# Kernel tuning notes

Hardware: AMD Instinct MI355X
Metric: run time of the kernel (lower is better)

Reference implementation:

```python
import jax, jax.numpy as jnp
import numpy as np

N_NODES = 10000
N_EDGES = 160000
D = 512            # input_dim = hidden_size = output_dim
NUM_EXPERTS = 4
N_LAYERS = 2


def setup_inputs() -> dict:
    key = jax.random.key(0)
    k = jax.random.split(key, 7)
    x = jax.random.normal(k[0], (N_NODES, D), dtype=jnp.float32)
    edge_index = jax.random.randint(k[1], (2, N_EDGES), 0, N_NODES, dtype=jnp.int32)
    # Gating network (Linear D -> NUM_EXPERTS)
    gate_w = jax.random.normal(k[2], (D, NUM_EXPERTS), dtype=jnp.float32) * 0.05
    gate_b = jnp.zeros((NUM_EXPERTS,), dtype=jnp.float32)
    # Per-expert SAGEConv weights: lin_r (self/root) and lin_l (neighbor) + bias
    w_self = jax.random.normal(k[3], (NUM_EXPERTS, N_LAYERS, D, D), dtype=jnp.float32) * 0.05
    w_neigh = jax.random.normal(k[4], (NUM_EXPERTS, N_LAYERS, D, D), dtype=jnp.float32) * 0.05
    b_exp = jnp.zeros((NUM_EXPERTS, N_LAYERS, D), dtype=jnp.float32)
    return {"x": x, "edge_index": edge_index, "gate_w": gate_w, "gate_b": gate_b,
            "w_self": w_self, "w_neigh": w_neigh, "b_exp": b_exp, "top_k": 1}


def reference(x, edge_index, gate_w, gate_b, w_self, w_neigh, b_exp, top_k):
    n = x.shape[0]
    src, dst = edge_index[0], edge_index[1]
    # mean-aggregation normalization (PyG SAGEConv aggr='mean'); 0 for isolated nodes
    deg = jax.ops.segment_sum(jnp.ones_like(src, dtype=x.dtype), dst, num_segments=n)
    inv_deg = jnp.where(deg > 0, 1.0 / jnp.maximum(deg, 1.0), 0.0)[:, None]  # [N,1]

    # gating: softmax(Linear(x)) then top-k routing
    gate = jax.nn.softmax(x @ gate_w + gate_b, axis=-1)          # [N, E]
    top_vals, top_idx = jax.lax.top_k(gate, top_k)               # [N, k]

    def expert(ws, wn, b):  # ws, wn: [L, D, D]; b: [L, D]
        h = x
        for l in range(N_LAYERS):
            agg = jax.ops.segment_sum(h[src], dst, num_segments=n) * inv_deg
            # SAGEConv: lin_l(mean_neigh) + lin_r(x) + bias, then relu (norm='id', eval dropout)
            h = jax.nn.relu(agg @ wn[l] + h @ ws[l] + b[l])
        return h

    # dense all-expert compute (matches original module)
    outs = jax.vmap(expert)(w_self, w_neigh, b_exp)              # [E, N, D]
    outs = jnp.transpose(outs, (1, 0, 2))                        # [N, E, D]
    sel = jnp.take_along_axis(outs, top_idx[:, :, None], axis=1)  # [N, k, D]
    return jnp.sum(sel * top_vals[:, :, None], axis=1)           # [N, D]
```

## Files before the change

### kernel.cpp

```cpp
#include <hip/hip_runtime.h>
#include <hip/hip_bf16.h>
#include <cstdint>

#define N_NODES 10000
#define N_EDGES 160000
#define DIM 512
#define K1 1024
#define NEXP 4

typedef __bf16 bf16_t;
typedef bf16_t bf16x8 __attribute__((ext_vector_type(8)));
typedef float f32x4 __attribute__((ext_vector_type(4)));

#define AS1(p) ((__attribute__((address_space(1))) void*)(p))
#define AS3(p) ((__attribute__((address_space(3))) void*)(p))

__global__ void zero_kernel(int* __restrict__ deg, int* __restrict__ ecnt) {
    int i = blockIdx.x * blockDim.x + threadIdx.x;
    if (i < N_NODES) deg[i] = 0;
    if (i < NEXP) ecnt[i] = 0;
}

__global__ void gate_kernel(const float* __restrict__ x,
                            const float* __restrict__ gw,
                            const float* __restrict__ gb,
                            int* __restrict__ top_idx,
                            float* __restrict__ top_val,
                            bf16_t* __restrict__ acat) {
    const int wave = threadIdx.x >> 6;
    const int lane = threadIdx.x & 63;
    const int node = blockIdx.x * 4 + wave;
    if (node >= N_NODES) return;
    const float4* x4 = (const float4*)(x + (size_t)node * DIM);
    const float4* gw4 = (const float4*)gw;
    float4 xa = x4[lane * 2];
    float4 xb = x4[lane * 2 + 1];
    float xv[8] = { xa.x, xa.y, xa.z, xa.w, xb.x, xb.y, xb.z, xb.w };
    float a0 = 0.f, a1 = 0.f, a2 = 0.f, a3 = 0.f;
    #pragma unroll
    for (int c = 0; c < 8; c++) {
        float4 g = gw4[lane * 8 + c];
        a0 += xv[c] * g.x; a1 += xv[c] * g.y; a2 += xv[c] * g.z; a3 += xv[c] * g.w;
    }
    bf16x8 o;
    #pragma unroll
    for (int c = 0; c < 8; c++) o[c] = (bf16_t)xv[c];
    *(bf16x8*)(acat + (size_t)node * K1 + DIM + lane * 8) = o;
    for (int off = 32; off > 0; off >>= 1) {
        a0 += __shfl_xor(a0, off);
        a1 += __shfl_xor(a1, off);
        a2 += __shfl_xor(a2, off);
        a3 += __shfl_xor(a3, off);
    }
    if (lane == 0) {
        float z[4] = { a0 + gb[0], a1 + gb[1], a2 + gb[2], a3 + gb[3] };
        int bi = 0; float bm = z[0];
        for (int e = 1; e < 4; e++) if (z[e] > bm) { bm = z[e]; bi = e; }
        float den = 0.f;
        for (int e = 0; e < 4; e++) den += expf(z[e] - bm);
        top_idx[node] = bi;
        top_val[node] = 1.0f / den;
    }
}

__global__ void bucket_kernel(const int* __restrict__ top_idx,
                              int* __restrict__ ecnt,
                              int* __restrict__ lists) {
    __shared__ int lcnt[NEXP];
    __shared__ int base[NEXP];
    const int tid = threadIdx.x;
    if (tid < NEXP) lcnt[tid] = 0;
    __syncthreads();
    const int node = blockIdx.x * 256 + tid;
    int e = 0, rank = 0;
    if (node < N_NODES) {
        e = top_idx[node];
        rank = atomicAdd(&lcnt[e], 1);
    }
    __syncthreads();
    if (tid < NEXP) base[tid] = atomicAdd(&ecnt[tid], lcnt[tid]);
    __syncthreads();
    if (node < N_NODES) lists[e * N_NODES + base[e] + rank] = node;
}

__global__ void deg_kernel(const int* __restrict__ dst, int* __restrict__ deg) {
    int i = blockIdx.x * blockDim.x + threadIdx.x;
    if (i < N_EDGES) atomicAdd(&deg[dst[i]], 1);
}

__global__ void scan_kernel(const int* __restrict__ deg,
                            int* __restrict__ offs,
                            int* __restrict__ cursor) {
    __shared__ int wsum[16];
    __shared__ int carrysh;
    const int tid = threadIdx.x;
    const int lane = tid & 63;
    const int wv = tid >> 6;
    if (tid == 0) carrysh = 0;
    __syncthreads();
    for (int base = 0; base < N_NODES; base += 1024) {
        int i = base + tid;
        int v = (i < N_NODES) ? deg[i] : 0;
        int s = v;
        #pragma unroll
        for (int off = 1; off < 64; off <<= 1) {
            int t = __shfl_up(s, off);
            if (lane >= off) s += t;
        }
        if (lane == 63) wsum[wv] = s;
        int carry = carrysh;
        __syncthreads();
        if (wv == 0) {
            int w = (lane < 16) ? wsum[lane] : 0;
            #pragma unroll
            for (int off = 1; off < 16; off <<= 1) {
                int t = __shfl_up(w, off);
                if (lane >= off) w += t;
            }
            if (lane < 16) wsum[lane] = w;
        }
        __syncthreads();
        int wbase = (wv > 0) ? wsum[wv - 1] : 0;
        int excl = carry + wbase + s - v;
        if (i < N_NODES) { offs[i] = excl; cursor[i] = excl; }
        int total = wsum[15];
        __syncthreads();
        if (tid == 0) carrysh = carry + total;
        __syncthreads();
    }
    if (tid == 0) offs[N_NODES] = carrysh;
}

__global__ void fill_kernel(const int* __restrict__ src, const int* __restrict__ dst,
                            int* __restrict__ cursor, int* __restrict__ csr) {
    int i = blockIdx.x * blockDim.x + threadIdx.x;
    if (i < N_EDGES) {
        int d = dst[i];
        int p = atomicAdd(&cursor[d], 1);
        csr[p] = src[i];
    }
}

__global__ void wtrans_kernel(const float* __restrict__ w_neigh,
                              const float* __restrict__ w_self,
                              bf16_t* __restrict__ Bt) {
    __shared__ float tile[32][33];
    const int m = blockIdx.z;
    const bool isSelf = m >= 8;
    const int el = m & 7;
    const float* W = (isSelf ? w_self : w_neigh) + (size_t)el * DIM * DIM;
    const int k0 = blockIdx.x * 32;
    const int n0 = blockIdx.y * 32;
    const int tx = threadIdx.x, ty = threadIdx.y;
    for (int r = ty; r < 32; r += 8)
        tile[r][tx] = W[(size_t)(k0 + r) * DIM + n0 + tx];
    __syncthreads();
    for (int r = ty; r < 32; r += 8) {
        int n = n0 + r;
        int k = k0 + tx;
        Bt[((size_t)el * DIM + n) * K1 + (isSelf ? DIM : 0) + k] = (bf16_t)tile[tx][r];
    }
}

__global__ void agg1_kernel(const int* __restrict__ offs, const int* __restrict__ csr,
                            bf16_t* __restrict__ acat) {
    const int wave = threadIdx.x >> 6;
    const int lane = threadIdx.x & 63;
    const int node = blockIdx.x * 4 + wave;
    if (node >= N_NODES) return;
    const int c0 = lane * 8;
    float s[8] = {0,0,0,0,0,0,0,0};
    int beg = offs[node];
    int end = offs[node + 1];
    int d = end - beg;
    int p = beg;
    for (; p + 8 <= end; p += 8) {
        bf16x8 v[8];
        #pragma unroll
        for (int q = 0; q < 8; q++) {
            int idx = csr[p + q];
            v[q] = *(const bf16x8*)(acat + (size_t)idx * K1 + DIM + c0);
        }
        #pragma unroll
        for (int q = 0; q < 8; q++)
            #pragma unroll
            for (int k = 0; k < 8; k++) s[k] += (float)v[q][k];
    }
    for (; p + 4 <= end; p += 4) {
        bf16x8 v[4];
        #pragma unroll
        for (int q = 0; q < 4; q++) {
            int idx = csr[p + q];
            v[q] = *(const bf16x8*)(acat + (size_t)idx * K1 + DIM + c0);
        }
        #pragma unroll
        for (int q = 0; q < 4; q++)
            #pragma unroll
            for (int k = 0; k < 8; k++) s[k] += (float)v[q][k];
    }
    for (; p < end; p++) {
        int idx = csr[p];
        bf16x8 v0 = *(const bf16x8*)(acat + (size_t)idx * K1 + DIM + c0);
        #pragma unroll
        for (int k = 0; k < 8; k++) s[k] += (float)v0[k];
    }
    float w = d > 0 ? 1.0f / (float)d : 0.0f;
    bf16x8 o;
    #pragma unroll
    for (int k = 0; k < 8; k++) o[k] = (bf16_t)(s[k] * w);
    *(bf16x8*)(acat + (size_t)node * K1 + c0) = o;
}

__global__ void agg2_kernel(const int* __restrict__ offs, const int* __restrict__ csr,
                            const int* __restrict__ top_idx,
                            const bf16_t* __restrict__ h1, bf16_t* __restrict__ acat) {
    const int wave = threadIdx.x >> 6;
    const int lane = threadIdx.x & 63;
    const int node = blockIdx.x * 4 + wave;
    if (node >= N_NODES) return;
    const int c0 = lane * 8;
    const bf16_t* hb = h1 + (size_t)top_idx[node] * N_NODES * DIM;
    float s[8] = {0,0,0,0,0,0,0,0};
    int beg = offs[node];
    int end = offs[node + 1];
    int d = end - beg;
    int p = beg;
    for (; p + 8 <= end; p += 8) {
        bf16x8 v[8];
        #pragma unroll
        for (int q = 0; q < 8; q++) {
            int idx = csr[p + q];
            v[q] = *(const bf16x8*)(hb + (size_t)idx * DIM + c0);
        }
        #pragma unroll
        for (int q = 0; q < 8; q++)
            #pragma unroll
            for (int k = 0; k < 8; k++) s[k] += (float)v[q][k];
    }
    for (; p + 4 <= end; p += 4) {
        bf16x8 v[4];
        #pragma unroll
        for (int q = 0; q < 4; q++) {
            int idx = csr[p + q];
            v[q] = *(const bf16x8*)(hb + (size_t)idx * DIM + c0);
        }
        #pragma unroll
        for (int q = 0; q < 4; q++)
            #pragma unroll
            for (int k = 0; k < 8; k++) s[k] += (float)v[q][k];
    }
    for (; p < end; p++) {
        int idx = csr[p];
        bf16x8 v0 = *(const bf16x8*)(hb + (size_t)idx * DIM + c0);
        #pragma unroll
        for (int k = 0; k < 8; k++) s[k] += (float)v0[k];
    }
    float w = d > 0 ? 1.0f / (float)d : 0.0f;
    bf16x8 o;
    #pragma unroll
    for (int k = 0; k < 8; k++) o[k] = (bf16_t)(s[k] * w);
    *(bf16x8*)(acat + (size_t)node * K1 + c0) = o;
    *(bf16x8*)(acat + (size_t)node * K1 + DIM + c0) = *(const bf16x8*)(hb + (size_t)node * DIM + c0);
}

template <int MODE>
__global__ __launch_bounds__(256)
void gemm_kernel(const bf16_t* __restrict__ A,
                 const bf16_t* __restrict__ Bt,
                 const int layer,
                 const float* __restrict__ bias_all,
                 bf16_t* __restrict__ h1,
                 float* __restrict__ out,
                 const int* __restrict__ lists,
                 const int* __restrict__ ecnt,
                 const float* __restrict__ top_val) {
    int bx, by, e;
    if (MODE == 0) {
        const int b = blockIdx.x;
        const int kq = b & 7;
        const int ke = kq >> 2;
        const int ky = kq & 3;
        const int r = b >> 3;
        const int yloc = r >> 3;
        const int xz = r & 7;
        bx = xz & 3;
        e = ke * 2 + (xz >> 2);
        by = ky * 20 + yloc;
        if (by >= 79) return;
    } else {
        bx = blockIdx.x; by = blockIdx.y; e = blockIdx.z;
    }
    int cnt = N_NODES;
    if (MODE == 1) {
        cnt = ecnt[e];
        if (by * 128 >= cnt) return;
    }
    __shared__ __align__(16) bf16_t As[128 * 32];
    __shared__ __align__(16) bf16_t Bs[128 * 32];

    const int t = threadIdx.x;
    const int lane = t & 63;
    const int wave = t >> 6;
    const int wm = wave >> 1;
    const int wn = wave & 1;

    const int r0 = t >> 2;
    const int rot = (t >> 3) & 3;
    const int cgl = ((t & 3) - rot) & 3;

    int i0 = by * 128 + r0;
    int i1 = i0 + 64;
    int arow0, arow1;
    if (MODE == 0) {
        arow0 = min(i0, N_NODES - 1);
        arow1 = min(i1, N_NODES - 1);
    } else {
        arow0 = lists[e * N_NODES + min(i0, cnt - 1)];
        arow1 = lists[e * N_NODES + min(i1, cnt - 1)];
    }
    const bf16_t* Bte = Bt + (size_t)(e * 2 + layer) * DIM * K1;
    const bf16_t* aptr0 = A + (size_t)arow0 * K1 + cgl * 8;
    const bf16_t* aptr1 = A + (size_t)arow1 * K1 + cgl * 8;
    const bf16_t* bptr0 = Bte + (size_t)(bx * 128 + r0) * K1 + cgl * 8;
    const bf16_t* bptr1 = bptr0 + (size_t)64 * K1;

    f32x4 acc[4][4] = {};
    char* asb = (char*)&As[0];
    char* bsb = (char*)&Bs[0];
    const int wb = wave * 1024;

    const int cpr = lane >> 4;
    const int rfr = lane & 15;

    for (int k0 = 0; k0 < K1; k0 += 32) {
        __syncthreads();
        __builtin_amdgcn_global_load_lds(AS1(aptr0), AS3(asb + wb),        16, 0, 0);
        __builtin_amdgcn_global_load_lds(AS1(aptr1), AS3(asb + 4096 + wb), 16, 0, 0);
        __builtin_amdgcn_global_load_lds(AS1(bptr0), AS3(bsb + wb),        16, 0, 0);
        __builtin_amdgcn_global_load_lds(AS1(bptr1), AS3(bsb + 4096 + wb), 16, 0, 0);
        __syncthreads();
        bf16x8 af[4], bfr[4];
        #pragma unroll
        for (int i = 0; i < 4; i++) {
            int r_full = wm * 64 + i * 16 + rfr;
            int p = (cpr + (r_full >> 1)) & 3;
            af[i] = *(const bf16x8*)(As + r_full * 32 + p * 8);
        }
        #pragma unroll
        for (int j = 0; j < 4; j++) {
            int r_full = wn * 64 + j * 16 + rfr;
            int p = (cpr + (r_full >> 1)) & 3;
            bfr[j] = *(const bf16x8*)(Bs + r_full * 32 + p * 8);
        }
        #pragma unroll
        for (int i = 0; i < 4; i++)
            #pragma unroll
            for (int j = 0; j < 4; j++)
                acc[i][j] = __builtin_amdgcn_mfma_f32_16x16x32_bf16(af[i], bfr[j], acc[i][j], 0, 0, 0);
        aptr0 += 32; aptr1 += 32; bptr0 += 32; bptr1 += 32;
    }

    const float* bias = bias_all + e * 1024 + layer * DIM;
    const int cbase = bx * 128 + wn * 64 + (lane & 15);
    float bv[4];
    #pragma unroll
    for (int j = 0; j < 4; j++) bv[j] = bias[cbase + j * 16];
    #pragma unroll
    for (int i = 0; i < 4; i++) {
        #pragma unroll
        for (int r = 0; r < 4; r++) {
            int row = by * 128 + wm * 64 + i * 16 + (lane >> 4) * 4 + r;
            if (MODE == 0) {
                if (row < N_NODES) {
                    bf16_t* cp = h1 + ((size_t)e * N_NODES + row) * DIM + cbase;
                    #pragma unroll
                    for (int j = 0; j < 4; j++) {
                        float v = fmaxf(acc[i][j][r] + bv[j], 0.f);
                        cp[j * 16] = (bf16_t)v;
                    }
                }
            } else {
                if (row < cnt) {
                    int node = lists[e * N_NODES + row];
                    float tv = top_val[node];
                    float* cp = out + (size_t)node * DIM + cbase;
                    #pragma unroll
                    for (int j = 0; j < 4; j++) {
                        float v = fmaxf(acc[i][j][r] + bv[j], 0.f);
                        cp[j * 16] = v * tv;
                    }
                }
            }
        }
    }
}

extern "C" void kernel_launch(void* const* d_in, const int* in_sizes, int n_in,
                              void* d_out, int out_size, void* d_ws, size_t ws_size,
                              hipStream_t stream) {
    const float* x       = (const float*)d_in[0];
    const int*   edge    = (const int*)d_in[1];
    const float* gw      = (const float*)d_in[2];
    const float* gb      = (const float*)d_in[3];
    const float* w_self  = (const float*)d_in[4];
    const float* w_neigh = (const float*)d_in[5];
    const float* b_exp   = (const float*)d_in[6];
    float* out = (float*)d_out;

    char* p = (char*)d_ws;
    auto alloc = [&](size_t bytes) {
        char* r = p;
        p += (bytes + 255) & ~(size_t)255;
        return r;
    };
    bf16_t* Bt      = (bf16_t*)alloc((size_t)8 * DIM * K1 * 2);
    bf16_t* acat    = (bf16_t*)alloc((size_t)N_NODES * K1 * 2);
    bf16_t* h1      = (bf16_t*)alloc((size_t)NEXP * N_NODES * DIM * 2);
    int*    deg     = (int*)alloc((size_t)N_NODES * 4);
    int*    offs    = (int*)alloc((size_t)(N_NODES + 1) * 4);
    int*    cursor  = (int*)alloc((size_t)N_NODES * 4);
    int*    csr     = (int*)alloc((size_t)N_EDGES * 4);
    int*    top_idx = (int*)alloc((size_t)N_NODES * 4);
    float*  top_val = (float*)alloc((size_t)N_NODES * 4);
    int*    ecnt    = (int*)alloc(256);
    int*    lists   = (int*)alloc((size_t)NEXP * N_NODES * 4);

    const int* srcE = edge;
    const int* dstE = edge + N_EDGES;

    zero_kernel<<<40, 256, 0, stream>>>(deg, ecnt);
    gate_kernel<<<N_NODES / 4, 256, 0, stream>>>(x, gw, gb, top_idx, top_val, acat);
    bucket_kernel<<<40, 256, 0, stream>>>(top_idx, ecnt, lists);
    deg_kernel<<<N_EDGES / 256, 256, 0, stream>>>(dstE, deg);
    scan_kernel<<<1, 1024, 0, stream>>>(deg, offs, cursor);
    fill_kernel<<<N_EDGES / 256, 256, 0, stream>>>(srcE, dstE, cursor, csr);
    wtrans_kernel<<<dim3(16, 16, 16), dim3(32, 8), 0, stream>>>(w_neigh, w_self, Bt);
    agg1_kernel<<<N_NODES / 4, 256, 0, stream>>>(offs, csr, acat);
    gemm_kernel<0><<<1280, 256, 0, stream>>>(acat, Bt, 0, b_exp, h1, nullptr, nullptr, nullptr, nullptr);
    agg2_kernel<<<N_NODES / 4, 256, 0, stream>>>(offs, csr, top_idx, h1, acat);
    gemm_kernel<1><<<dim3(4, 79, 4), 256, 0, stream>>>(acat, Bt, 1, b_exp, nullptr, out, lists, ecnt, top_val);
}
```

Measured before the change: 276.5 us.

## Compute two experts per block in layer-1 GEMM to reuse shared A tile

The layer-1 GEMM now assigns each block two experts that share the same A (aggregated+self features) tile. The A tile is loaded once into LDS and multiplied against two B tiles, which halves A global traffic and the block count (1280 to 640). The cost is doubled accumulator registers (128 floats), which may lower occupancy or cause spills, and fewer blocks to fill the CUs. The templated GEMM is split into two specialised kernels.

```diff
diff --git a/kernel.cpp b/kernel.cpp
--- a/kernel.cpp
+++ b/kernel.cpp
@@ -263,40 +263,23 @@
     *(bf16x8*)(acat + (size_t)node * K1 + DIM + c0) = *(const bf16x8*)(hb + (size_t)node * DIM + c0);
 }
 
-template <int MODE>
 __global__ __launch_bounds__(256)
-void gemm_kernel(const bf16_t* __restrict__ A,
-                 const bf16_t* __restrict__ Bt,
-                 const int layer,
-                 const float* __restrict__ bias_all,
-                 bf16_t* __restrict__ h1,
-                 float* __restrict__ out,
-                 const int* __restrict__ lists,
-                 const int* __restrict__ ecnt,
-                 const float* __restrict__ top_val) {
-    int bx, by, e;
-    if (MODE == 0) {
-        const int b = blockIdx.x;
-        const int kq = b & 7;
-        const int ke = kq >> 2;
-        const int ky = kq & 3;
-        const int r = b >> 3;
-        const int yloc = r >> 3;
-        const int xz = r & 7;
-        bx = xz & 3;
-        e = ke * 2 + (xz >> 2);
-        by = ky * 20 + yloc;
-        if (by >= 79) return;
-    } else {
-        bx = blockIdx.x; by = blockIdx.y; e = blockIdx.z;
-    }
-    int cnt = N_NODES;
-    if (MODE == 1) {
-        cnt = ecnt[e];
-        if (by * 128 >= cnt) return;
-    }
+void gemm1_kernel(const bf16_t* __restrict__ A,
+                  const bf16_t* __restrict__ Bt,
+                  const float* __restrict__ bias_all,
+                  bf16_t* __restrict__ h1) {
+    const int b = blockIdx.x;
+    const int xcd = b & 7;
+    const int ep = xcd >> 2;
+    const int yq = xcd & 3;
+    const int r = b >> 3;
+    const int yloc = r >> 2;
+    const int bx = r & 3;
+    const int by = yq * 20 + yloc;
+    if (by >= 79) return;
+
     __shared__ __align__(16) bf16_t As[128 * 32];
-    __shared__ __align__(16) bf16_t Bs[128 * 32];
+    __shared__ __align__(16) bf16_t Bs[2][128 * 32];
 
     const int t = threadIdx.x;
     const int lane = t & 63;
@@ -310,15 +293,120 @@
 
     int i0 = by * 128 + r0;
     int i1 = i0 + 64;
-    int arow0, arow1;
-    if (MODE == 0) {
-        arow0 = min(i0, N_NODES - 1);
-        arow1 = min(i1, N_NODES - 1);
-    } else {
-        arow0 = lists[e * N_NODES + min(i0, cnt - 1)];
-        arow1 = lists[e * N_NODES + min(i1, cnt - 1)];
-    }
-    const bf16_t* Bte = Bt + (size_t)(e * 2 + layer) * DIM * K1;
+    int arow0 = min(i0, N_NODES - 1);
+    int arow1 = min(i1, N_NODES - 1);
+
+    const bf16_t* aptr0 = A + (size_t)arow0 * K1 + cgl * 8;
+    const bf16_t* aptr1 = A + (size_t)arow1 * K1 + cgl * 8;
+    const int e0 = ep * 2;
+    const bf16_t* Bt0 = Bt + (size_t)(e0 * 2) * DIM * K1;
+    const bf16_t* Bt1 = Bt + (size_t)((e0 + 1) * 2) * DIM * K1;
+    const bf16_t* bptr00 = Bt0 + (size_t)(bx * 128 + r0) * K1 + cgl * 8;
+    const bf16_t* bptr01 = bptr00 + (size_t)64 * K1;
+    const bf16_t* bptr10 = Bt1 + (size_t)(bx * 128 + r0) * K1 + cgl * 8;
+    const bf16_t* bptr11 = bptr10 + (size_t)64 * K1;
+
+    f32x4 acc[2][4][4] = {};
+    char* asb = (char*)&As[0];
+    char* bsb0 = (char*)&Bs[0][0];
+    char* bsb1 = (char*)&Bs[1][0];
+    const int wb = wave * 1024;
+
+    const int cpr = lane >> 4;
+    const int rfr = lane & 15;
+
+    for (int k0 = 0; k0 < K1; k0 += 32) {
+        __syncthreads();
+        __builtin_amdgcn_global_load_lds(AS1(aptr0),  AS3(asb + wb),         16, 0, 0);
+        __builtin_amdgcn_global_load_lds(AS1(aptr1),  AS3(asb + 4096 + wb),  16, 0, 0);
+        __builtin_amdgcn_global_load_lds(AS1(bptr00), AS3(bsb0 + wb),        16, 0, 0);
+        __builtin_amdgcn_global_load_lds(AS1(bptr01), AS3(bsb0 + 4096 + wb), 16, 0, 0);
+        __builtin_amdgcn_global_load_lds(AS1(bptr10), AS3(bsb1 + wb),        16, 0, 0);
+        __builtin_amdgcn_global_load_lds(AS1(bptr11), AS3(bsb1 + 4096 + wb), 16, 0, 0);
+        __syncthreads();
+        bf16x8 af[4];
+        #pragma unroll
+        for (int i = 0; i < 4; i++) {
+            int rf = wm * 64 + i * 16 + rfr;
+            int pp = (cpr + (rf >> 1)) & 3;
+            af[i] = *(const bf16x8*)(As + rf * 32 + pp * 8);
+        }
+        #pragma unroll
+        for (int u = 0; u < 2; u++) {
+            bf16x8 bfr[4];
+            #pragma unroll
+            for (int j = 0; j < 4; j++) {
+                int rf = wn * 64 + j * 16 + rfr;
+                int pp = (cpr + (rf >> 1)) & 3;
+                bfr[j] = *(const bf16x8*)(&Bs[u][0] + rf * 32 + pp * 8);
+            }
+            #pragma unroll
+            for (int i = 0; i < 4; i++)
+                #pragma unroll
+                for (int j = 0; j < 4; j++)
+                    acc[u][i][j] = __builtin_amdgcn_mfma_f32_16x16x32_bf16(af[i], bfr[j], acc[u][i][j], 0, 0, 0);
+        }
+        aptr0 += 32; aptr1 += 32;
+        bptr00 += 32; bptr01 += 32; bptr10 += 32; bptr11 += 32;
+    }
+
+    const int cbase = bx * 128 + wn * 64 + (lane & 15);
+    #pragma unroll
+    for (int u = 0; u < 2; u++) {
+        const int e = e0 + u;
+        const float* bias = bias_all + e * 1024;
+        float bv[4];
+        #pragma unroll
+        for (int j = 0; j < 4; j++) bv[j] = bias[cbase + j * 16];
+        #pragma unroll
+        for (int i = 0; i < 4; i++) {
+            #pragma unroll
+            for (int rr = 0; rr < 4; rr++) {
+                int row = by * 128 + wm * 64 + i * 16 + (lane >> 4) * 4 + rr;
+                if (row < N_NODES) {
+                    bf16_t* cp = h1 + ((size_t)e * N_NODES + row) * DIM + cbase;
+                    #pragma unroll
+                    for (int j = 0; j < 4; j++) {
+                        float v = fmaxf(acc[u][i][j][rr] + bv[j], 0.f);
+                        cp[j * 16] = (bf16_t)v;
+                    }
+                }
+            }
+        }
+    }
+}
+
+__global__ __launch_bounds__(256)
+void gemm2_kernel(const bf16_t* __restrict__ A,
+                  const bf16_t* __restrict__ Bt,
+                  const float* __restrict__ bias_all,
+                  float* __restrict__ out,
+                  const int* __restrict__ lists,
+                  const int* __restrict__ ecnt,
+                  const float* __restrict__ top_val) {
+    const int bx = blockIdx.x, by = blockIdx.y, e = blockIdx.z;
+    const int cnt = ecnt[e];
+    if (by * 128 >= cnt) return;
+
+    __shared__ __align__(16) bf16_t As[128 * 32];
+    __shared__ __align__(16) bf16_t Bs[128 * 32];
+
+    const int t = threadIdx.x;
+    const int lane = t & 63;
+    const int wave = t >> 6;
+    const int wm = wave >> 1;
+    const int wn = wave & 1;
+
+    const int r0 = t >> 2;
+    const int rot = (t >> 3) & 3;
+    const int cgl = ((t & 3) - rot) & 3;
+
+    int i0 = by * 128 + r0;
+    int i1 = i0 + 64;
+    int arow0 = lists[e * N_NODES + min(i0, cnt - 1)];
+    int arow1 = lists[e * N_NODES + min(i1, cnt - 1)];
+
+    const bf16_t* Bte = Bt + (size_t)(e * 2 + 1) * DIM * K1;
     const bf16_t* aptr0 = A + (size_t)arow0 * K1 + cgl * 8;
     const bf16_t* aptr1 = A + (size_t)arow1 * K1 + cgl * 8;
     const bf16_t* bptr0 = Bte + (size_t)(bx * 128 + r0) * K1 + cgl * 8;
@@ -342,15 +430,15 @@
         bf16x8 af[4], bfr[4];
         #pragma unroll
         for (int i = 0; i < 4; i++) {
-            int r_full = wm * 64 + i * 16 + rfr;
-            int p = (cpr + (r_full >> 1)) & 3;
-            af[i] = *(const bf16x8*)(As + r_full * 32 + p * 8);
+            int rf = wm * 64 + i * 16 + rfr;
+            int pp = (cpr + (rf >> 1)) & 3;
+            af[i] = *(const bf16x8*)(As + rf * 32 + pp * 8);
         }
         #pragma unroll
         for (int j = 0; j < 4; j++) {
-            int r_full = wn * 64 + j * 16 + rfr;
-            int p = (cpr + (r_full >> 1)) & 3;
-            bfr[j] = *(const bf16x8*)(Bs + r_full * 32 + p * 8);
+            int rf = wn * 64 + j * 16 + rfr;
+            int pp = (cpr + (rf >> 1)) & 3;
+            bfr[j] = *(const bf16x8*)(Bs + rf * 32 + pp * 8);
         }
         #pragma unroll
         for (int i = 0; i < 4; i++)
@@ -360,7 +448,7 @@
         aptr0 += 32; aptr1 += 32; bptr0 += 32; bptr1 += 32;
     }
 
-    const float* bias = bias_all + e * 1024 + layer * DIM;
+    const float* bias = bias_all + e * 1024 + DIM;
     const int cbase = bx * 128 + wn * 64 + (lane & 15);
     float bv[4];
     #pragma unroll
@@ -368,27 +456,16 @@
     #pragma unroll
     for (int i = 0; i < 4; i++) {
         #pragma unroll
-        for (int r = 0; r < 4; r++) {
-            int row = by * 128 + wm * 64 + i * 16 + (lane >> 4) * 4 + r;
-            if (MODE == 0) {
-                if (row < N_NODES) {
-                    bf16_t* cp = h1 + ((size_t)e * N_NODES + row) * DIM + cbase;
-                    #pragma unroll
-                    for (int j = 0; j < 4; j++) {
-                        float v = fmaxf(acc[i][j][r] + bv[j], 0.f);
-                        cp[j * 16] = (bf16_t)v;
-                    }
-                }
-            } else {
-                if (row < cnt) {
-                    int node = lists[e * N_NODES + row];
-                    float tv = top_val[node];
-                    float* cp = out + (size_t)node * DIM + cbase;
-                    #pragma unroll
-                    for (int j = 0; j < 4; j++) {
-                        float v = fmaxf(acc[i][j][r] + bv[j], 0.f);
-                        cp[j * 16] = v * tv;
-                    }
+        for (int rr = 0; rr < 4; rr++) {
+            int row = by * 128 + wm * 64 + i * 16 + (lane >> 4) * 4 + rr;
+            if (row < cnt) {
+                int node = lists[e * N_NODES + row];
+                float tv = top_val[node];
+                float* cp = out + (size_t)node * DIM + cbase;
+                #pragma unroll
+                for (int j = 0; j < 4; j++) {
+                    float v = fmaxf(acc[i][j][rr] + bv[j], 0.f);
+                    cp[j * 16] = v * tv;
                 }
             }
         }
@@ -436,7 +513,7 @@
     fill_kernel<<<N_EDGES / 256, 256, 0, stream>>>(srcE, dstE, cursor, csr);
     wtrans_kernel<<<dim3(16, 16, 16), dim3(32, 8), 0, stream>>>(w_neigh, w_self, Bt);
     agg1_kernel<<<N_NODES / 4, 256, 0, stream>>>(offs, csr, acat);
-    gemm_kernel<0><<<1280, 256, 0, stream>>>(acat, Bt, 0, b_exp, h1, nullptr, nullptr, nullptr, nullptr);
+    gemm1_kernel<<<640, 256, 0, stream>>>(acat, Bt, b_exp, h1);
     agg2_kernel<<<N_NODES / 4, 256, 0, stream>>>(offs, csr, top_idx, h1, acat);
-    gemm_kernel<1><<<dim3(4, 79, 4), 256, 0, stream>>>(acat, Bt, 1, b_exp, nullptr, out, lists, ecnt, top_val);
-}
+    gemm2_kernel<<<dim3(4, 79, 4), 256, 0, stream>>>(acat, Bt, b_exp, out, lists, ecnt, top_val);
+}
```

Result: slower. 332.7 us (+20.3%).
